# Kernel tuning notes

Measured on AMD Instinct MI355X. Metric: run time of the kernel, lower is better.

The kernel has to match this reference:

```python
import jax, jax.numpy as jnp
import numpy as np

B, C, H, W = 2, 1024, 64, 64
E, TOP_K = 8, 2
FFN = C  # ffn_dim = in_channels; hidden_dim = out_channels = in_channels


def setup_inputs() -> dict:
    key = jax.random.key(0)
    ks = jax.random.split(key, 5)
    s = 0.02
    return {
        "hidden_states": jax.random.normal(ks[0], (B, C, H, W), jnp.float32),
        "gate_w": jax.random.normal(ks[1], (E, C), jnp.float32) * s,   # torch Linear weight [out,in]
        "w1": jax.random.normal(ks[2], (E, FFN, C), jnp.float32) * s,
        "w2": jax.random.normal(ks[3], (E, C, FFN), jnp.float32) * s,
        "w3": jax.random.normal(ks[4], (E, FFN, C), jnp.float32) * s,
    }


def reference(hidden_states, gate_w, w1, w2, w3):
    b, c = hidden_states.shape[0], hidden_states.shape[1]
    space = hidden_states.shape[2:]
    # (B, C, H, W) -> (B, H, W, C) -> (T, C)
    x = jnp.transpose(hidden_states, (0, 2, 3, 1)).reshape(-1, c)

    # Router: softmax in float32, top-k, renormalize (matches torch)
    logits = x @ gate_w.T                                   # [T, E]
    probs = jax.nn.softmax(logits.astype(jnp.float32), axis=-1)
    rw, sel = jax.lax.top_k(probs, TOP_K)                   # [T, K]
    rw = rw / jnp.sum(rw, axis=-1, keepdims=True)
    rw = rw.astype(x.dtype)

    # Combine weights per expert: zero where expert not selected -> exact
    # equivalence with gather/scatter dispatch (full capacity, no drops).
    combine = jnp.sum(jax.nn.one_hot(sel, E, dtype=x.dtype) * rw[..., None], axis=1)  # [T, E]

    out = jnp.zeros_like(x)
    for e in range(E):  # small fixed expert loop
        h = jax.nn.gelu(x @ w1[e].T, approximate=False) * (x @ w3[e].T)  # SwiGLU-style [T, FFN]
        out = out + combine[:, e:e + 1] * (h @ w2[e].T)

    out = out.reshape(b, *space, c)
    return jnp.transpose(out, (0, 3, 1, 2))  # (B, C, H, W)
```

## Files before the change

### kernel.cpp

```cpp
#include <hip/hip_runtime.h>
#include <hip/hip_bf16.h>
#include <math.h>

#define BB 2
#define CC 1024
#define HH 64
#define WW 64
#define HWH (HH*WW)
#define TT (BB*HWH)
#define EE 8
#define FFN 1024
#define HCAP 17408
#define MAXTILES 136

typedef __bf16 bf16x8 __attribute__((ext_vector_type(8)));
typedef __bf16 bf16x4 __attribute__((ext_vector_type(4)));
typedef float  f32x4  __attribute__((ext_vector_type(4)));

__device__ __forceinline__ void gl_lds16(const __bf16* g, __bf16* l) {
    __builtin_amdgcn_global_load_lds(
        (const __attribute__((address_space(1))) void*)g,
        (__attribute__((address_space(3))) void*)l, 16, 0, 0);
}

__device__ __forceinline__ void barrier_raw() {
    asm volatile("" ::: "memory");
    __builtin_amdgcn_s_barrier();
    asm volatile("" ::: "memory");
}

#define CVB 12288
#define XPB 8192
#define RTB 512
__global__ __launch_bounds__(256) void k_prep(
    const float* __restrict__ hs, const float* __restrict__ gate_w,
    const float* __restrict__ w1, const float* __restrict__ w2,
    const float* __restrict__ w3,
    __bf16* __restrict__ w1b, __bf16* __restrict__ w2b,
    __bf16* __restrict__ w3b, __bf16* __restrict__ X,
    float* __restrict__ logP) {
    __shared__ float sm[2112];
    const int bid = blockIdx.x;
    const int tid = threadIdx.x;

    if (bid < CVB) {
        const float* s; __bf16* d; int lb = bid;
        if (lb < 4096)      { s = w1; d = w1b; }
        else if (lb < 8192) { s = w2; d = w2b; lb -= 4096; }
        else                { s = w3; d = w3b; lb -= 8192; }
        const size_t i = (size_t)lb * 2048 + (size_t)tid * 8;
        const f32x4 v0 = *(const f32x4*)&s[i];
        const f32x4 v1 = *(const f32x4*)&s[i + 4];
        bf16x8 o;
#pragma unroll
        for (int j = 0; j < 4; ++j) { o[j] = (__bf16)v0[j]; o[4 + j] = (__bf16)v1[j]; }
        *(bf16x8*)&d[i] = o;
    } else if (bid < CVB + XPB) {
        const int lb  = bid - CVB;
        const int hw0 = (lb & 127) * 32;
        const int c0  = ((lb >> 7) & 31) * 32;
        const int b   = lb >> 12;
        float (*tile)[33] = (float(*)[33])sm;
        const int tx = tid & 31, ty = tid >> 5;
        const float* src = hs + ((size_t)b * CC + c0) * HWH + hw0;
#pragma unroll
        for (int i = 0; i < 4; ++i)
            tile[ty + i * 8][tx] = src[(size_t)(ty + i * 8) * HWH + tx];
        __syncthreads();
        __bf16* dst = X + ((size_t)b * HWH + hw0) * CC + c0;
#pragma unroll
        for (int i = 0; i < 4; ++i) {
            const int hwl = ty + i * 8;
            dst[(size_t)hwl * CC + tx] = (__bf16)tile[tx][hwl];
        }
    } else {
        const int lb  = bid - (CVB + XPB);
        const int q   = lb & 3;
        const int t64 = lb >> 2;
        float* g = sm;
        for (int i = tid; i < 2048; i += 256)
            g[i] = gate_w[(size_t)(i >> 8) * CC + q * 256 + (i & 255)];
        __syncthreads();
        const int q2 = tid >> 6, tl = tid & 63;
        const int t  = t64 * 64 + tl;
        const int b  = t >> 12, hw = t & 4095;
        const float* xp = hs + (size_t)b * CC * HWH + hw;
        float l[EE];
#pragma unroll
        for (int e = 0; e < EE; ++e) l[e] = 0.0f;
        const int cbase = q * 256 + q2 * 64;
        for (int c2 = 0; c2 < 64; ++c2) {
            const float xv = xp[(size_t)(cbase + c2) * HWH];
#pragma unroll
            for (int e = 0; e < EE; ++e) l[e] += xv * g[e * 256 + q2 * 64 + c2];
        }
        float* dst = logP + ((size_t)(q * 4 + q2) * TT + t) * 8;
        f32x4 a, c;
#pragma unroll
        for (int e = 0; e < 4; ++e) { a[e] = l[e]; c[e] = l[4 + e]; }
        *(f32x4*)dst = a;
        *(f32x4*)&dst[4] = c;
    }
}

__global__ __launch_bounds__(256) void k_top2(const float* __restrict__ logP,
                                              int* __restrict__ cnt,
                                              int* __restrict__ idxl,
                                              int* __restrict__ tokE,
                                              int* __restrict__ tokP,
                                              float* __restrict__ tokW) {
    __shared__ int lcnt[EE], lbase[EE];
    const int tid = threadIdx.x;
    const int t   = blockIdx.x * 256 + tid;
    if (tid < EE) lcnt[tid] = 0;
    __syncthreads();

    float l[EE];
#pragma unroll
    for (int e = 0; e < EE; ++e) l[e] = 0.0f;
#pragma unroll
    for (int pq = 0; pq < 16; ++pq) {
        const float* src = logP + ((size_t)pq * TT + t) * 8;
        const f32x4 a = *(const f32x4*)src;
        const f32x4 c = *(const f32x4*)&src[4];
#pragma unroll
        for (int e = 0; e < 4; ++e) { l[e] += a[e]; l[4 + e] += c[e]; }
    }

    int e1 = 0; float v1 = l[0];
#pragma unroll
    for (int e = 1; e < EE; ++e) { if (l[e] > v1) { v1 = l[e]; e1 = e; } }
    int e2 = -1; float v2 = -1e30f;
#pragma unroll
    for (int e = 0; e < EE; ++e) { if (e != e1 && l[e] > v2) { v2 = l[e]; e2 = e; } }

    const float p2 = __expf(v2 - v1);
    const float rs = 1.0f / (1.0f + p2);

    const int m1 = atomicAdd(&lcnt[e1], 1);
    const int m2 = atomicAdd(&lcnt[e2], 1);
    __syncthreads();
    if (tid < EE) lbase[tid] = atomicAdd(&cnt[tid], lcnt[tid]);
    __syncthreads();
    const int p1pos = lbase[e1] + m1;
    const int p2pos = lbase[e2] + m2;

    idxl[e1 * TT + p1pos] = t;
    idxl[e2 * TT + p2pos] = t;
    tokE[t] = e1 | (e2 << 8);
    tokP[2 * t]     = p1pos;
    tokP[2 * t + 1] = p2pos;
    tokW[2 * t]     = rs;
    tokW[2 * t + 1] = p2 * rs;
}

__global__ void k_offsets(const int* __restrict__ cnt, int* __restrict__ off,
                          int* __restrict__ tileE, int* __restrict__ tileM,
                          int* __restrict__ nT) {
    if (threadIdx.x == 0) {
        int a = 0, n = 0;
        for (int e = 0; e < EE; ++e) {
            off[e] = a;
            const int mt = (cnt[e] + 127) >> 7;
            for (int m = 0; m < mt; ++m) { tileE[n] = e; tileM[n] = m * 128; ++n; }
            a += mt * 128;
        }
        nT[0] = n;
    }
}

__global__ __launch_bounds__(256, 2)
void k_gemm1(const __bf16* __restrict__ X, const __bf16* __restrict__ w1b,
             const __bf16* __restrict__ w3b, const int* __restrict__ cnt,
             const int* __restrict__ off, const int* __restrict__ idxl,
             const int* __restrict__ tileE, const int* __restrict__ tileM,
             const int* __restrict__ nT, __bf16* __restrict__ H) {
    if ((int)blockIdx.y >= nT[0]) return;
    const int e     = tileE[blockIdx.y];
    const int mt128 = tileM[blockIdx.y];
    const int cntE  = cnt[e];
    const int goff  = off[e];
    const int n0    = blockIdx.x * 128;
    const __bf16* W1 = w1b + (size_t)e * FFN * CC;
    const __bf16* W3 = w3b + (size_t)e * FFN * CC;

    __shared__ __bf16 sA[2][128 * 32];
    __shared__ __bf16 sB1[2][128 * 32];
    __shared__ __bf16 sB3[2][128 * 32];

    const int tid  = threadIdx.x;
    const int lane = tid & 63;
    const int wave = tid >> 6;
    const int wm   = (wave & 1) * 64;
    const int wn   = (wave >> 1) * 64;
    const int l15  = lane & 15;
    const int lq   = lane >> 4;
    const int rl   = lane >> 2;
    const int cpos = lane & 3;
    const int c8s = (cpos ^ ((rl >> 1) & 3)) * 8;
    const int cq  = ((lq ^ ((l15 >> 1) & 3))) * 8;

    int p0 = mt128 + wave * 32 + rl;      if (p0 > cntE - 1) p0 = cntE - 1;
    int p1 = mt128 + wave * 32 + 16 + rl; if (p1 > cntE - 1) p1 = cntE - 1;
    const __bf16* ga0  = X + (size_t)idxl[e * TT + p0] * CC + c8s;
    const __bf16* ga1  = X + (size_t)idxl[e * TT + p1] * CC + c8s;
    const __bf16* gb10 = W1 + (size_t)(n0 + wave * 32 + rl) * CC + c8s;
    const __bf16* gb11 = W1 + (size_t)(n0 + wave * 32 + 16 + rl) * CC + c8s;
    const __bf16* gb30 = W3 + (size_t)(n0 + wave * 32 + rl) * CC + c8s;
    const __bf16* gb31 = W3 + (size_t)(n0 + wave * 32 + 16 + rl) * CC + c8s;
    const int lofs0 = (wave * 32) * 32;
    const int lofs1 = (wave * 32 + 16) * 32;

    f32x4 acc1[4][4] = {};
    f32x4 acc3[4][4] = {};

    auto stage = [&](int b, int kb) {
        gl_lds16(ga0 + kb,  &sA[b][lofs0]);
        gl_lds16(ga1 + kb,  &sA[b][lofs1]);
        gl_lds16(gb10 + kb, &sB1[b][lofs0]);
        gl_lds16(gb11 + kb, &sB1[b][lofs1]);
        gl_lds16(gb30 + kb, &sB3[b][lofs0]);
        gl_lds16(gb31 + kb, &sB3[b][lofs1]);
    };

    stage(0, 0);
    int p = 0;
    for (int kb = 0; kb < CC; kb += 32, p ^= 1) {
        if (kb + 32 < CC) {
            stage(p ^ 1, kb + 32);
            asm volatile("s_waitcnt vmcnt(6)" ::: "memory");
        } else {
            asm volatile("s_waitcnt vmcnt(0)" ::: "memory");
        }
        barrier_raw();

        bf16x8 af[4], b1f[4], b3f[4];
#pragma unroll
        for (int i = 0; i < 4; ++i)
            af[i] = *(const bf16x8*)&sA[p][(wm + i * 16 + l15) * 32 + cq];
#pragma unroll
        for (int j = 0; j < 4; ++j)
            b1f[j] = *(const bf16x8*)&sB1[p][(wn + j * 16 + l15) * 32 + cq];
#pragma unroll
        for (int j = 0; j < 4; ++j)
            b3f[j] = *(const bf16x8*)&sB3[p][(wn + j * 16 + l15) * 32 + cq];
        asm volatile("s_waitcnt lgkmcnt(0)" ::: "memory");
        barrier_raw();

#pragma unroll
        for (int i = 0; i < 4; ++i)
#pragma unroll
            for (int j = 0; j < 4; ++j) {
                acc1[i][j] = __builtin_amdgcn_mfma_f32_16x16x32_bf16(
                    af[i], b1f[j], acc1[i][j], 0, 0, 0);
                acc3[i][j] = __builtin_amdgcn_mfma_f32_16x16x32_bf16(
                    af[i], b3f[j], acc3[i][j], 0, 0, 0);
            }
    }

#pragma unroll
    for (int i = 0; i < 4; ++i) {
        const int gb = goff + mt128 + wm + i * 16 + lq * 4;
#pragma unroll
        for (int j = 0; j < 4; ++j) {
            const int nb = n0 + wn + j * 16 + l15;
#pragma unroll
            for (int r = 0; r < 4; ++r) {
                const float a  = acc1[i][j][r];
                const float c  = acc3[i][j][r];
                const float ge = 0.5f * a * (1.0f + erff(a * 0.70710678118654752f));
                H[(size_t)(gb + r) * FFN + nb] = (__bf16)(ge * c);
            }
        }
    }
}

__global__ __launch_bounds__(256, 2)
void k_gemm2(const __bf16* __restrict__ H, const __bf16* __restrict__ w2b,
             const int* __restrict__ off, const int* __restrict__ tileE,
             const int* __restrict__ tileM, const int* __restrict__ nT,
             __bf16* __restrict__ Z) {
    if ((int)blockIdx.y >= nT[0]) return;
    const int e     = tileE[blockIdx.y];
    const int mt128 = tileM[blockIdx.y];
    const int goff  = off[e];
    const int n0    = blockIdx.x * 128;
    const __bf16* W2 = w2b + (size_t)e * CC * FFN;
    const __bf16* Arows = H + (size_t)(goff + mt128) * FFN;

    __shared__ __bf16 sA[2][128 * 32];
    __shared__ __bf16 sB[2][128 * 32];

    const int tid  = threadIdx.x;
    const int lane = tid & 63;
    const int wave = tid >> 6;
    const int wm   = (wave & 1) * 64;
    const int wn   = (wave >> 1) * 64;
    const int l15  = lane & 15;
    const int lq   = lane >> 4;
    const int rl   = lane >> 2;
    const int cpos = lane & 3;
    const int c8s = (cpos ^ ((rl >> 1) & 3)) * 8;
    const int cq  = ((lq ^ ((l15 >> 1) & 3))) * 8;

    const __bf16* ga0 = Arows + (size_t)(wave * 32 + rl) * FFN + c8s;
    const __bf16* ga1 = Arows + (size_t)(wave * 32 + 16 + rl) * FFN + c8s;
    const __bf16* gb0 = W2 + (size_t)(n0 + wave * 32 + rl) * FFN + c8s;
    const __bf16* gb1 = W2 + (size_t)(n0 + wave * 32 + 16 + rl) * FFN + c8s;
    const int lofs0 = (wave * 32) * 32;
    const int lofs1 = (wave * 32 + 16) * 32;

    f32x4 acc[4][4] = {};

    auto stage = [&](int b, int kb) {
        gl_lds16(ga0 + kb, &sA[b][lofs0]);
        gl_lds16(ga1 + kb, &sA[b][lofs1]);
        gl_lds16(gb0 + kb, &sB[b][lofs0]);
        gl_lds16(gb1 + kb, &sB[b][lofs1]);
    };

    stage(0, 0);
    int p = 0;
    for (int kb = 0; kb < FFN; kb += 32, p ^= 1) {
        if (kb + 32 < FFN) {
            stage(p ^ 1, kb + 32);
            asm volatile("s_waitcnt vmcnt(4)" ::: "memory");
        } else {
            asm volatile("s_waitcnt vmcnt(0)" ::: "memory");
        }
        barrier_raw();

        bf16x8 af[4], bf[4];
#pragma unroll
        for (int i = 0; i < 4; ++i)
            af[i] = *(const bf16x8*)&sA[p][(wm + i * 16 + l15) * 32 + cq];
#pragma unroll
        for (int j = 0; j < 4; ++j)
            bf[j] = *(const bf16x8*)&sB[p][(wn + j * 16 + l15) * 32 + cq];
        asm volatile("s_waitcnt lgkmcnt(0)" ::: "memory");
        barrier_raw();

#pragma unroll
        for (int i = 0; i < 4; ++i)
#pragma unroll
            for (int j = 0; j < 4; ++j)
                acc[i][j] = __builtin_amdgcn_mfma_f32_16x16x32_bf16(
                    af[i], bf[j], acc[i][j], 0, 0, 0);
    }

#pragma unroll
    for (int i = 0; i < 4; ++i) {
        const int gb = goff + mt128 + wm + i * 16 + lq * 4;
#pragma unroll
        for (int j = 0; j < 4; ++j) {
            const int c = n0 + wn + j * 16 + l15;
#pragma unroll
            for (int r = 0; r < 4; ++r)
                Z[(size_t)(gb + r) * CC + c] = (__bf16)acc[i][j][r];
        }
    }
}

__global__ __launch_bounds__(256) void k_combine(const __bf16* __restrict__ Z,
                                                 const int* __restrict__ off,
                                                 const int* __restrict__ tokE,
                                                 const int* __restrict__ tokP,
                                                 const float* __restrict__ tokW,
                                                 float* __restrict__ out) {
    __shared__ float tile[32][33];
    const int t0 = blockIdx.x * 32;
    const int c0 = blockIdx.y * 32;
    const int tx = threadIdx.x & 31;
    const int ty = threadIdx.x >> 5;

#pragma unroll
    for (int i = 0; i < 4; ++i) {
        const int tl = ty + 8 * i;
        const int t  = t0 + tl;
        const int ee = tokE[t];
        const int e1 = ee & 0xff, e2 = ee >> 8;
        const int r1 = off[e1] + tokP[2 * t];
        const int r2 = off[e2] + tokP[2 * t + 1];
        const float v = tokW[2 * t]     * (float)Z[(size_t)r1 * CC + c0 + tx]
                      + tokW[2 * t + 1] * (float)Z[(size_t)r2 * CC + c0 + tx];
        tile[tl][tx] = v;
    }
    __syncthreads();

    const int b   = t0 >> 12;
    const int hw0 = t0 & 4095;
#pragma unroll
    for (int i = 0; i < 4; ++i) {
        const int cl = ty + 8 * i;
        out[(size_t)b * CC * HWH + (size_t)(c0 + cl) * HWH + hw0 + tx] = tile[tx][cl];
    }
}

extern "C" void kernel_launch(void* const* d_in, const int* in_sizes, int n_in,
                              void* d_out, int out_size, void* d_ws, size_t ws_size,
                              hipStream_t stream) {
    const float* hs     = (const float*)d_in[0];
    const float* gate_w = (const float*)d_in[1];
    const float* w1     = (const float*)d_in[2];
    const float* w2     = (const float*)d_in[3];
    const float* w3     = (const float*)d_in[4];
    float* out = (float*)d_out;

    const size_t WSZ = (size_t)EE * FFN * CC * 2;
    char* ws = (char*)d_ws;
    __bf16* w2b  = (__bf16*)ws;
    __bf16* w1b  = (__bf16*)(ws + WSZ);
    __bf16* w3b  = (__bf16*)(ws + 2 * WSZ);
    __bf16* X    = (__bf16*)(ws + 3 * WSZ);
    __bf16* Zbuf = (__bf16*)(ws + WSZ);
    __bf16* Hbuf = (__bf16*)(ws + 4 * WSZ);
    float*  logP = (float*)Hbuf;
    char* p = ws + 4 * WSZ + (size_t)HCAP * FFN * 2;
    int*   idxl  = (int*)p;           p += (size_t)EE * TT * 4;
    int*   tokE  = (int*)p;           p += (size_t)TT * 4;
    int*   tokP  = (int*)p;           p += (size_t)2 * TT * 4;
    float* tokW  = (float*)p;         p += (size_t)2 * TT * 4;
    int*   cnt   = (int*)p;           p += 256;
    int*   off   = (int*)p;           p += 256;
    int*   tileE = (int*)p;           p += MAXTILES * 4;
    int*   tileM = (int*)p;           p += MAXTILES * 4;
    int*   nT    = (int*)p;

    hipMemsetAsync(cnt, 0, EE * sizeof(int), stream);

    k_prep<<<CVB + XPB + RTB, 256, 0, stream>>>(
        hs, gate_w, w1, w2, w3, w1b, w2b, w3b, X, logP);
    k_top2<<<TT / 256, 256, 0, stream>>>(logP, cnt, idxl, tokE, tokP, tokW);
    k_offsets<<<1, 64, 0, stream>>>(cnt, off, tileE, tileM, nT);

    k_gemm1<<<dim3(FFN / 128, MAXTILES), 256, 0, stream>>>(
        X, w1b, w3b, cnt, off, idxl, tileE, tileM, nT, Hbuf);
    k_gemm2<<<dim3(CC / 128, MAXTILES), 256, 0, stream>>>(
        Hbuf, w2b, off, tileE, tileM, nT, Zbuf);
    k_combine<<<dim3(TT / 32, CC / 32), 256, 0, stream>>>(
        Zbuf, off, tokE, tokP, tokW, out);
}
```

Before: 374.7 us.

## Load GEMM A operands directly to registers and fold routing weights into gemm2

Both grouped GEMMs stop staging the A operand (gathered tokens or hidden rows) through LDS and load it straight from global memory into registers, prefetching one k-step ahead. B stays double-buffered in LDS, and the second barrier per iteration is dropped. The routing weight is stored per expert position and applied in the gemm2 epilogue, so combine becomes a plain sum. Launch bounds rise to 3 blocks per CU, using the freed LDS, at the cost of register pressure and uncoalesced per-lane A loads. Rows past the expert count in a tile read posW entries that top2 never writes, so padding rows may carry garbage weights into unused Z rows.

```diff
diff --git a/kernel.cpp b/kernel.cpp
--- a/kernel.cpp
+++ b/kernel.cpp
@@ -28,6 +28,7 @@
     __builtin_amdgcn_s_barrier();
     asm volatile("" ::: "memory");
 }
+__device__ __forceinline__ void memfence() { asm volatile("" ::: "memory"); }
 
 #define CVB 12288
 #define XPB 8192
@@ -108,7 +109,7 @@
                                               int* __restrict__ idxl,
                                               int* __restrict__ tokE,
                                               int* __restrict__ tokP,
-                                              float* __restrict__ tokW) {
+                                              float* __restrict__ posW) {
     __shared__ int lcnt[EE], lbase[EE];
     const int tid = threadIdx.x;
     const int t   = blockIdx.x * 256 + tid;
@@ -147,11 +148,11 @@
 
     idxl[e1 * TT + p1pos] = t;
     idxl[e2 * TT + p2pos] = t;
+    posW[e1 * TT + p1pos] = rs;
+    posW[e2 * TT + p2pos] = p2 * rs;
     tokE[t] = e1 | (e2 << 8);
     tokP[2 * t]     = p1pos;
     tokP[2 * t + 1] = p2pos;
-    tokW[2 * t]     = rs;
-    tokW[2 * t + 1] = p2 * rs;
 }
 
 __global__ void k_offsets(const int* __restrict__ cnt, int* __restrict__ off,
@@ -169,7 +170,7 @@
     }
 }
 
-__global__ __launch_bounds__(256, 2)
+__global__ __launch_bounds__(256, 3)
 void k_gemm1(const __bf16* __restrict__ X, const __bf16* __restrict__ w1b,
              const __bf16* __restrict__ w3b, const int* __restrict__ cnt,
              const int* __restrict__ off, const int* __restrict__ idxl,
@@ -184,7 +185,6 @@
     const __bf16* W1 = w1b + (size_t)e * FFN * CC;
     const __bf16* W3 = w3b + (size_t)e * FFN * CC;
 
-    __shared__ __bf16 sA[2][128 * 32];
     __shared__ __bf16 sB1[2][128 * 32];
     __shared__ __bf16 sB3[2][128 * 32];
 
@@ -198,12 +198,15 @@
     const int rl   = lane >> 2;
     const int cpos = lane & 3;
     const int c8s = (cpos ^ ((rl >> 1) & 3)) * 8;
-    const int cq  = ((lq ^ ((l15 >> 1) & 3))) * 8;
-
-    int p0 = mt128 + wave * 32 + rl;      if (p0 > cntE - 1) p0 = cntE - 1;
-    int p1 = mt128 + wave * 32 + 16 + rl; if (p1 > cntE - 1) p1 = cntE - 1;
-    const __bf16* ga0  = X + (size_t)idxl[e * TT + p0] * CC + c8s;
-    const __bf16* ga1  = X + (size_t)idxl[e * TT + p1] * CC + c8s;
+    const int cq  = (lq ^ ((l15 >> 1) & 3)) * 8;
+
+    const __bf16* arow[4];
+#pragma unroll
+    for (int i = 0; i < 4; ++i) {
+        int pos = mt128 + wm + i * 16 + l15;
+        if (pos > cntE - 1) pos = cntE - 1;
+        arow[i] = X + (size_t)idxl[e * TT + pos] * CC + lq * 8;
+    }
     const __bf16* gb10 = W1 + (size_t)(n0 + wave * 32 + rl) * CC + c8s;
     const __bf16* gb11 = W1 + (size_t)(n0 + wave * 32 + 16 + rl) * CC + c8s;
     const __bf16* gb30 = W3 + (size_t)(n0 + wave * 32 + rl) * CC + c8s;
@@ -213,49 +216,56 @@
 
     f32x4 acc1[4][4] = {};
     f32x4 acc3[4][4] = {};
-
-    auto stage = [&](int b, int kb) {
-        gl_lds16(ga0 + kb,  &sA[b][lofs0]);
-        gl_lds16(ga1 + kb,  &sA[b][lofs1]);
+    bf16x8 aCur[4], aNxt[4];
+
+    auto stageB = [&](int b, int kb) {
         gl_lds16(gb10 + kb, &sB1[b][lofs0]);
         gl_lds16(gb11 + kb, &sB1[b][lofs1]);
         gl_lds16(gb30 + kb, &sB3[b][lofs0]);
         gl_lds16(gb31 + kb, &sB3[b][lofs1]);
     };
-
-    stage(0, 0);
+    auto loadA = [&](bf16x8* a, int kb) {
+#pragma unroll
+        for (int i = 0; i < 4; ++i) a[i] = *(const bf16x8*)&arow[i][kb];
+    };
+
+    stageB(0, 0);
+    memfence();
+    loadA(aCur, 0);
+    memfence();
+
     int p = 0;
     for (int kb = 0; kb < CC; kb += 32, p ^= 1) {
-        if (kb + 32 < CC) {
-            stage(p ^ 1, kb + 32);
-            asm volatile("s_waitcnt vmcnt(6)" ::: "memory");
-        } else {
-            asm volatile("s_waitcnt vmcnt(0)" ::: "memory");
-        }
+        asm volatile("s_waitcnt vmcnt(4)" ::: "memory");
         barrier_raw();
 
-        bf16x8 af[4], b1f[4], b3f[4];
-#pragma unroll
-        for (int i = 0; i < 4; ++i)
-            af[i] = *(const bf16x8*)&sA[p][(wm + i * 16 + l15) * 32 + cq];
+        bf16x8 b1f[4], b3f[4];
 #pragma unroll
         for (int j = 0; j < 4; ++j)
             b1f[j] = *(const bf16x8*)&sB1[p][(wn + j * 16 + l15) * 32 + cq];
 #pragma unroll
         for (int j = 0; j < 4; ++j)
             b3f[j] = *(const bf16x8*)&sB3[p][(wn + j * 16 + l15) * 32 + cq];
-        asm volatile("s_waitcnt lgkmcnt(0)" ::: "memory");
-        barrier_raw();
+
+        if (kb + 32 < CC) {
+            memfence();
+            stageB(p ^ 1, kb + 32);
+            memfence();
+            loadA(aNxt, kb + 32);
+            memfence();
+        }
 
 #pragma unroll
         for (int i = 0; i < 4; ++i)
 #pragma unroll
             for (int j = 0; j < 4; ++j) {
                 acc1[i][j] = __builtin_amdgcn_mfma_f32_16x16x32_bf16(
-                    af[i], b1f[j], acc1[i][j], 0, 0, 0);
+                    aCur[i], b1f[j], acc1[i][j], 0, 0, 0);
                 acc3[i][j] = __builtin_amdgcn_mfma_f32_16x16x32_bf16(
-                    af[i], b3f[j], acc3[i][j], 0, 0, 0);
+                    aCur[i], b3f[j], acc3[i][j], 0, 0, 0);
             }
+#pragma unroll
+        for (int i = 0; i < 4; ++i) aCur[i] = aNxt[i];
     }
 
 #pragma unroll
@@ -275,20 +285,18 @@
     }
 }
 
-__global__ __launch_bounds__(256, 2)
+__global__ __launch_bounds__(256, 3)
 void k_gemm2(const __bf16* __restrict__ H, const __bf16* __restrict__ w2b,
              const int* __restrict__ off, const int* __restrict__ tileE,
              const int* __restrict__ tileM, const int* __restrict__ nT,
-             __bf16* __restrict__ Z) {
+             const float* __restrict__ posW, __bf16* __restrict__ Z) {
     if ((int)blockIdx.y >= nT[0]) return;
     const int e     = tileE[blockIdx.y];
     const int mt128 = tileM[blockIdx.y];
     const int goff  = off[e];
     const int n0    = blockIdx.x * 128;
     const __bf16* W2 = w2b + (size_t)e * CC * FFN;
-    const __bf16* Arows = H + (size_t)(goff + mt128) * FFN;
-
-    __shared__ __bf16 sA[2][128 * 32];
+
     __shared__ __bf16 sB[2][128 * 32];
 
     const int tid  = threadIdx.x;
@@ -301,62 +309,73 @@
     const int rl   = lane >> 2;
     const int cpos = lane & 3;
     const int c8s = (cpos ^ ((rl >> 1) & 3)) * 8;
-    const int cq  = ((lq ^ ((l15 >> 1) & 3))) * 8;
-
-    const __bf16* ga0 = Arows + (size_t)(wave * 32 + rl) * FFN + c8s;
-    const __bf16* ga1 = Arows + (size_t)(wave * 32 + 16 + rl) * FFN + c8s;
+    const int cq  = (lq ^ ((l15 >> 1) & 3)) * 8;
+
+    const __bf16* arow[4];
+#pragma unroll
+    for (int i = 0; i < 4; ++i)
+        arow[i] = H + (size_t)(goff + mt128 + wm + i * 16 + l15) * FFN + lq * 8;
     const __bf16* gb0 = W2 + (size_t)(n0 + wave * 32 + rl) * FFN + c8s;
     const __bf16* gb1 = W2 + (size_t)(n0 + wave * 32 + 16 + rl) * FFN + c8s;
     const int lofs0 = (wave * 32) * 32;
     const int lofs1 = (wave * 32 + 16) * 32;
 
     f32x4 acc[4][4] = {};
-
-    auto stage = [&](int b, int kb) {
-        gl_lds16(ga0 + kb, &sA[b][lofs0]);
-        gl_lds16(ga1 + kb, &sA[b][lofs1]);
+    bf16x8 aCur[4], aNxt[4];
+
+    auto stageB = [&](int b, int kb) {
         gl_lds16(gb0 + kb, &sB[b][lofs0]);
         gl_lds16(gb1 + kb, &sB[b][lofs1]);
     };
-
-    stage(0, 0);
+    auto loadA = [&](bf16x8* a, int kb) {
+#pragma unroll
+        for (int i = 0; i < 4; ++i) a[i] = *(const bf16x8*)&arow[i][kb];
+    };
+
+    stageB(0, 0);
+    memfence();
+    loadA(aCur, 0);
+    memfence();
+
     int p = 0;
     for (int kb = 0; kb < FFN; kb += 32, p ^= 1) {
-        if (kb + 32 < FFN) {
-            stage(p ^ 1, kb + 32);
-            asm volatile("s_waitcnt vmcnt(4)" ::: "memory");
-        } else {
-            asm volatile("s_waitcnt vmcnt(0)" ::: "memory");
-        }
+        asm volatile("s_waitcnt vmcnt(4)" ::: "memory");
         barrier_raw();
 
-        bf16x8 af[4], bf[4];
-#pragma unroll
-        for (int i = 0; i < 4; ++i)
-            af[i] = *(const bf16x8*)&sA[p][(wm + i * 16 + l15) * 32 + cq];
+        bf16x8 bf[4];
 #pragma unroll
         for (int j = 0; j < 4; ++j)
             bf[j] = *(const bf16x8*)&sB[p][(wn + j * 16 + l15) * 32 + cq];
-        asm volatile("s_waitcnt lgkmcnt(0)" ::: "memory");
-        barrier_raw();
+
+        if (kb + 32 < FFN) {
+            memfence();
+            stageB(p ^ 1, kb + 32);
+            memfence();
+            loadA(aNxt, kb + 32);
+            memfence();
+        }
 
 #pragma unroll
         for (int i = 0; i < 4; ++i)
 #pragma unroll
             for (int j = 0; j < 4; ++j)
                 acc[i][j] = __builtin_amdgcn_mfma_f32_16x16x32_bf16(
-                    af[i], bf[j], acc[i][j], 0, 0, 0);
+                    aCur[i], bf[j], acc[i][j], 0, 0, 0);
+#pragma unroll
+        for (int i = 0; i < 4; ++i) aCur[i] = aNxt[i];
     }
 
 #pragma unroll
     for (int i = 0; i < 4; ++i) {
-        const int gb = goff + mt128 + wm + i * 16 + lq * 4;
+        const int pos = mt128 + wm + i * 16 + lq * 4;
+        const int gb  = goff + pos;
+        const f32x4 wrow = *(const f32x4*)&posW[e * TT + pos];
 #pragma unroll
         for (int j = 0; j < 4; ++j) {
             const int c = n0 + wn + j * 16 + l15;
 #pragma unroll
             for (int r = 0; r < 4; ++r)
-                Z[(size_t)(gb + r) * CC + c] = (__bf16)acc[i][j][r];
+                Z[(size_t)(gb + r) * CC + c] = (__bf16)(acc[i][j][r] * wrow[r]);
         }
     }
 }
@@ -365,7 +384,6 @@
                                                  const int* __restrict__ off,
                                                  const int* __restrict__ tokE,
                                                  const int* __restrict__ tokP,
-                                                 const float* __restrict__ tokW,
                                                  float* __restrict__ out) {
     __shared__ float tile[32][33];
     const int t0 = blockIdx.x * 32;
@@ -381,9 +399,8 @@
         const int e1 = ee & 0xff, e2 = ee >> 8;
         const int r1 = off[e1] + tokP[2 * t];
         const int r2 = off[e2] + tokP[2 * t + 1];
-        const float v = tokW[2 * t]     * (float)Z[(size_t)r1 * CC + c0 + tx]
-                      + tokW[2 * t + 1] * (float)Z[(size_t)r2 * CC + c0 + tx];
-        tile[tl][tx] = v;
+        tile[tl][tx] = (float)Z[(size_t)r1 * CC + c0 + tx]
+                     + (float)Z[(size_t)r2 * CC + c0 + tx];
     }
     __syncthreads();
 
@@ -419,7 +436,7 @@
     int*   idxl  = (int*)p;           p += (size_t)EE * TT * 4;
     int*   tokE  = (int*)p;           p += (size_t)TT * 4;
     int*   tokP  = (int*)p;           p += (size_t)2 * TT * 4;
-    float* tokW  = (float*)p;         p += (size_t)2 * TT * 4;
+    float* posW  = (float*)p;         p += (size_t)EE * TT * 4;
     int*   cnt   = (int*)p;           p += 256;
     int*   off   = (int*)p;           p += 256;
     int*   tileE = (int*)p;           p += MAXTILES * 4;
@@ -430,13 +447,13 @@
 
     k_prep<<<CVB + XPB + RTB, 256, 0, stream>>>(
         hs, gate_w, w1, w2, w3, w1b, w2b, w3b, X, logP);
-    k_top2<<<TT / 256, 256, 0, stream>>>(logP, cnt, idxl, tokE, tokP, tokW);
+    k_top2<<<TT / 256, 256, 0, stream>>>(logP, cnt, idxl, tokE, tokP, posW);
     k_offsets<<<1, 64, 0, stream>>>(cnt, off, tileE, tileM, nT);
 
     k_gemm1<<<dim3(FFN / 128, MAXTILES), 256, 0, stream>>>(
         X, w1b, w3b, cnt, off, idxl, tileE, tileM, nT, Hbuf);
     k_gemm2<<<dim3(CC / 128, MAXTILES), 256, 0, stream>>>(
-        Hbuf, w2b, off, tileE, tileM, nT, Zbuf);
+        Hbuf, w2b, off, tileE, tileM, nT, posW, Zbuf);
     k_combine<<<dim3(TT / 32, CC / 32), 256, 0, stream>>>(
-        Zbuf, off, tokE, tokP, tokW, out);
-}
+        Zbuf, off, tokE, tokP, out);
+}
```

Result: slower. 874.6 us (+133.4%).
